# Performance work log

Measured on AMD Instinct MI355X. Metric: run time of the kernel, lower is better.

## Reference

```python
import jax, jax.numpy as jnp
import numpy as np

ALPHA = 0.34          # Ewald splitting parameter (init kwarg alpha)
MAX_HKL = 12          # init kwarg max_hkl
TWO_PI = 2.0 * np.pi


def setup_inputs() -> dict:
    key = jax.random.key(0)
    k1, k2 = jax.random.split(key)
    N = 4096
    L = 40.0  # cubic box edge (Angstrom)
    coords = jax.random.uniform(k1, (N, 3), dtype=jnp.float32) * L
    q = jax.random.normal(k2, (N,), dtype=jnp.float32)
    q = q - jnp.mean(q)  # neutral cell (k=0 term is excluded)
    box = jnp.eye(3, dtype=jnp.float32) * L
    return {"coords": coords, "box": box, "q": q}


def _ewald_recip_energy(coords, box, q):
    """Reciprocal-space Ewald sum over |h|,|k|,|l| <= MAX_HKL (rank=0 PME fallback).

    pot_i = (4*pi/V) * sum_{k!=0} exp(-|k|^2/(4 a^2))/|k|^2 * Re[S(k) exp(-i k.r_i)]
    E     = 0.5 * sum_i q_i * pot_i
    """
    K = MAX_HKL
    vol = jnp.abs(jnp.linalg.det(box))
    recip = TWO_PI * jnp.linalg.inv(box).T  # rows = reciprocal lattice vectors (3,3)
    h = jnp.arange(-K, K + 1)
    hh, kk, ll = jnp.meshgrid(h, h, h, indexing="ij")
    hkl = jnp.stack([hh.ravel(), kk.ravel(), ll.ravel()], axis=-1).astype(jnp.float32)  # (Nk,3)
    kvecs = hkl @ recip                      # (Nk,3)
    k2 = jnp.sum(kvecs * kvecs, axis=-1)     # (Nk,)
    nonzero = k2 > 0.0                       # mask out k = 0 (static shape, jit-safe)
    k2_safe = jnp.where(nonzero, k2, 1.0)
    inv_4a2 = 1.0 / (4.0 * ALPHA * ALPHA)
    fac = jnp.where(nonzero, jnp.exp(-k2_safe * inv_4a2) / k2_safe, 0.0)  # (Nk,)
    phases = coords @ kvecs.T                # (N, Nk)
    c = jnp.cos(phases)
    s = jnp.sin(phases)
    Sre = q @ c                              # (Nk,) Re S(k)
    Sim = q @ s                              # (Nk,) Im S(k)
    pref = (4.0 * np.pi) / vol
    # Re[S(k) e^{-i k.r_i}] = Sre*cos + Sim*sin
    pot = pref * (c @ (fac * Sre) + s @ (fac * Sim))  # (N,)
    return 0.5 * jnp.sum(q * pot)


def reference(coords, box, q):
    return _ewald_recip_energy(coords, box, q)
```

## Files before the change

kernel.cpp:

```cpp
#include <hip/hip_runtime.h>
#include <math.h>

namespace {
constexpr int   KMAX   = 12;
constexpr int   NLINE  = 313;
constexpr int   NGROUP = NLINE * 5;
constexpr int   NKV    = NGROUP * 5;
constexpr int   NSLICE = 4;
constexpr int   SLICE_CAP = 512;
constexpr int   S2_BLOCKS = (NKV + 255) / 256;
constexpr float ALPHA_  = 0.34f;
constexpr float TWO_PI_ = 6.283185307179586f;
}

__device__ __forceinline__ void cofactors(const float* __restrict__ box,
                                          float C[3][3], float* det) {
  const float b00 = box[0], b01 = box[1], b02 = box[2];
  const float b10 = box[3], b11 = box[4], b12 = box[5];
  const float b20 = box[6], b21 = box[7], b22 = box[8];
  C[0][0] =  (b11 * b22 - b12 * b21);
  C[0][1] = -(b10 * b22 - b12 * b20);
  C[0][2] =  (b10 * b21 - b11 * b20);
  C[1][0] = -(b01 * b22 - b02 * b21);
  C[1][1] =  (b00 * b22 - b02 * b20);
  C[1][2] = -(b00 * b21 - b01 * b20);
  C[2][0] =  (b01 * b12 - b02 * b11);
  C[2][1] = -(b00 * b12 - b02 * b10);
  C[2][2] =  (b00 * b11 - b01 * b10);
  *det = b00 * C[0][0] + b01 * C[0][1] + b02 * C[0][2];
}

__device__ __forceinline__ void line_hk(int L, int* h, int* k) {
  if (L < 300)      { *h = L / 25 + 1; *k = L % 25 - 12; }
  else if (L < 312) { *h = 0;          *k = L - 299;     }
  else              { *h = 0;          *k = 0;           }
}

__global__ __launch_bounds__(256, 6) void ewald_g5(
    const float* __restrict__ coords, const float* __restrict__ box,
    const float* __restrict__ q, int N, float2* __restrict__ partial)
{
  __shared__ float4 sf4[SLICE_CAP];
  __shared__ float2 sf2[SLICE_CAP];

  float C[3][3], det;
  cofactors(box, C, &det);
  const float invdet = 1.0f / det;

  const int slice = blockIdx.y;
  const int sp    = (N + NSLICE - 1) / NSLICE;
  const int s_beg = slice * sp;
  const int s_end = min(s_beg + sp, N);

  const int lane = threadIdx.x & 63;
  const int g    = blockIdx.x * 4 + (threadIdx.x >> 6);
  const int gc   = (g < NGROUP) ? g : (NGROUP - 1);

  int h, k; line_hk(gc / 5, &h, &k);
  const float hf  = (float)h;
  const float kf  = (float)k;
  const float l0f = (float)(-KMAX + 5 * (gc % 5));

  float Sre[5] = {0.f, 0.f, 0.f, 0.f, 0.f};
  float Sim[5] = {0.f, 0.f, 0.f, 0.f, 0.f};

  for (int cb = s_beg; cb < s_end; cb += SLICE_CAP) {
    const int cnt = min(SLICE_CAP, s_end - cb);
    __syncthreads();
    for (int t = threadIdx.x; t < SLICE_CAP; t += 256) {
      float4 v4 = make_float4(0.f, 0.f, 1.f, 0.f);
      float2 v2 = make_float2(0.f, 0.f);
      if (t < cnt) {
        const int gi = cb + t;
        const float x = coords[3 * gi + 0];
        const float y = coords[3 * gi + 1];
        const float z = coords[3 * gi + 2];
        v4.x = (x * C[0][0] + y * C[0][1] + z * C[0][2]) * invdet;
        v4.y = (x * C[1][0] + y * C[1][1] + z * C[1][2]) * invdet;
        float c = (x * C[2][0] + y * C[2][1] + z * C[2][2]) * invdet;
        c = c - floorf(c);
        float cr, sr;
        asm("v_sin_f32 %0, %1" : "=v"(sr) : "v"(c));
        asm("v_cos_f32 %0, %1" : "=v"(cr) : "v"(c));
        v4.z = cr; v4.w = sr;
        v2.x = c;  v2.y = q[gi];
      }
      sf4[t] = v4; sf2[t] = v2;
    }
    __syncthreads();

#pragma unroll 2
    for (int i = lane; i < SLICE_CAP; i += 64) {
      const float4 p = sf4[i];
      const float2 w = sf2[i];
      float t0 = fmaf(hf, p.x, fmaf(kf, p.y, l0f * w.x));
      float tf;
      asm("v_fract_f32 %0, %1" : "=v"(tf) : "v"(t0));
      float s0, c0;
      asm("v_sin_f32 %0, %1" : "=v"(s0) : "v"(tf));
      asm("v_cos_f32 %0, %1" : "=v"(c0) : "v"(tf));
      float Pre = w.y * c0, Pim = w.y * s0;
      Sre[0] += Pre; Sim[0] += Pim;
      const float cr = p.z, sr = p.w;
#pragma unroll
      for (int u = 1; u < 5; ++u) {
        const float nre = fmaf(Pre, cr, -(Pim * sr));
        const float nim = fmaf(Pre, sr,  (Pim * cr));
        Pre = nre; Pim = nim;
        Sre[u] += Pre; Sim[u] += Pim;
      }
    }
  }

#pragma unroll
  for (int off = 32; off > 0; off >>= 1) {
#pragma unroll
    for (int u = 0; u < 5; ++u) {
      Sre[u] += __shfl_xor(Sre[u], off);
      Sim[u] += __shfl_xor(Sim[u], off);
    }
  }

  if (g < NGROUP && lane == 0) {
#pragma unroll
    for (int u = 0; u < 5; ++u) {
      partial[(size_t)(g * 5 + u) * NSLICE + slice] = make_float2(Sre[u], Sim[u]);
    }
  }
}

__global__ __launch_bounds__(256) void stage2(
    const float2* __restrict__ partial, const float* __restrict__ box,
    float* __restrict__ out)
{
  __shared__ float red[256];
  const int idx = blockIdx.x * 256 + threadIdx.x;
  float e = 0.f;
  if (idx < NKV) {
    const int g = idx / 5, u = idx % 5;
    const int line = g / 5;
    const int l = -KMAX + 5 * (g % 5) + u;
    int h, k; line_hk(line, &h, &k);
    if (!(h == 0 && k == 0 && l <= 0)) {
      float re = 0.f, im = 0.f;
      for (int s = 0; s < NSLICE; ++s) {
        const float2 p = partial[(size_t)idx * NSLICE + s];
        re += p.x; im += p.y;
      }
      float C[3][3], det;
      cofactors(box, C, &det);
      const float invdet = 1.0f / det;
      const float hf = (float)h, kf = (float)k, lf = (float)l;
      const float kx = (hf * C[0][0] + kf * C[1][0] + lf * C[2][0]) * invdet;
      const float ky = (hf * C[0][1] + kf * C[1][1] + lf * C[2][1]) * invdet;
      const float kz = (hf * C[0][2] + kf * C[1][2] + lf * C[2][2]) * invdet;
      const float k2 = TWO_PI_ * TWO_PI_ * (kx * kx + ky * ky + kz * kz);
      const float fac = __expf(-k2 / (4.0f * ALPHA_ * ALPHA_)) / k2;
      e = fac * fmaf(re, re, im * im);
    }
  }
  red[threadIdx.x] = e;
  __syncthreads();
  for (int s = 128; s > 0; s >>= 1) {
    if (threadIdx.x < s) red[threadIdx.x] += red[threadIdx.x + s];
    __syncthreads();
  }
  if (threadIdx.x == 0) {
    float C[3][3], det;
    cofactors(box, C, &det);
    const float scale = (4.0f * 3.14159265358979323846f) / fabsf(det);
    atomicAdd(out, scale * red[0]);
  }
}

extern "C" void kernel_launch(void* const* d_in, const int* in_sizes, int n_in,
                              void* d_out, int out_size, void* d_ws, size_t ws_size,
                              hipStream_t stream) {
  const float* coords = (const float*)d_in[0];
  const float* box    = (const float*)d_in[1];
  const float* q      = (const float*)d_in[2];
  float* out = (float*)d_out;
  const int N = in_sizes[2];

  float2* partial = (float2*)d_ws;

  hipMemsetAsync(out, 0, sizeof(float), stream);
  const dim3 grid((NGROUP + 3) / 4, NSLICE);
  hipLaunchKernelGGL(ewald_g5, grid, dim3(256), 0, stream,
                     coords, box, q, N, partial);
  hipLaunchKernelGGL(stage2, dim3(S2_BLOCKS), dim3(256), 0, stream,
                     partial, box, out);
}
```

Before: 24.15 us.

## Map one k-group per thread with 128 atom slices, dropping wave reductions

The work split changes. Before, each wave handled one k-group over a quarter of the atoms and finished with a cross-lane shuffle reduction. Now each thread owns one k-group and each block handles a slice of 32 atoms, for 128 slices. Per-thread partials are written to the workspace, and stage2 reduces across the 128 slices using 4 lanes per k-vector. The hipMemsetAsync is replaced by an in-kernel zero of the output, which removes a launch but relies on the first kernel finishing before stage2's atomics. The cost is much more partial-sum traffic, about 128×7825 float2 values, plus a heavier stage2 reduction.

```diff
diff --git a/kernel.cpp b/kernel.cpp
--- a/kernel.cpp
+++ b/kernel.cpp
@@ -4,11 +4,13 @@
 namespace {
 constexpr int   KMAX   = 12;
 constexpr int   NLINE  = 313;
-constexpr int   NGROUP = NLINE * 5;
-constexpr int   NKV    = NGROUP * 5;
-constexpr int   NSLICE = 4;
-constexpr int   SLICE_CAP = 512;
-constexpr int   S2_BLOCKS = (NKV + 255) / 256;
+constexpr int   NL25   = 25;
+constexpr int   NKV    = NLINE * NL25;
+constexpr int   NG     = NLINE * 5;
+constexpr int   GPAD   = 7 * 256;
+constexpr int   NSLICE = 128;
+constexpr int   PART   = 32;
+constexpr int   S2_BLOCKS = (NKV * 4 + 255) / 256;
 constexpr float ALPHA_  = 0.34f;
 constexpr float TWO_PI_ = 6.283185307179586f;
 }
@@ -36,96 +38,79 @@
   else              { *h = 0;          *k = 0;           }
 }
 
-__global__ __launch_bounds__(256, 6) void ewald_g5(
+__global__ __launch_bounds__(256, 8) void ewald_t(
     const float* __restrict__ coords, const float* __restrict__ box,
-    const float* __restrict__ q, int N, float2* __restrict__ partial)
+    const float* __restrict__ q, int N, float2* __restrict__ partial,
+    float* __restrict__ out)
 {
-  __shared__ float4 sf4[SLICE_CAP];
-  __shared__ float2 sf2[SLICE_CAP];
-
-  float C[3][3], det;
-  cofactors(box, C, &det);
-  const float invdet = 1.0f / det;
+  __shared__ float4 sf4[PART];
+  __shared__ float2 sf2[PART];
 
   const int slice = blockIdx.y;
-  const int sp    = (N + NSLICE - 1) / NSLICE;
-  const int s_beg = slice * sp;
-  const int s_end = min(s_beg + sp, N);
+  if (blockIdx.x == 0 && slice == 0 && threadIdx.x == 0) out[0] = 0.0f;
 
-  const int lane = threadIdx.x & 63;
-  const int g    = blockIdx.x * 4 + (threadIdx.x >> 6);
-  const int gc   = (g < NGROUP) ? g : (NGROUP - 1);
+  if (threadIdx.x < PART) {
+    float C[3][3], det;
+    cofactors(box, C, &det);
+    const float invdet = 1.0f / det;
+    const int i = slice * PART + threadIdx.x;
+    float4 v4 = make_float4(0.f, 0.f, 1.f, 0.f);
+    float2 v2 = make_float2(0.f, 0.f);
+    if (i < N) {
+      const float x = coords[3 * i + 0];
+      const float y = coords[3 * i + 1];
+      const float z = coords[3 * i + 2];
+      v4.x = (x * C[0][0] + y * C[0][1] + z * C[0][2]) * invdet;
+      v4.y = (x * C[1][0] + y * C[1][1] + z * C[1][2]) * invdet;
+      float c = (x * C[2][0] + y * C[2][1] + z * C[2][2]) * invdet;
+      c = c - floorf(c);
+      float cr, sr;
+      asm("v_sin_f32 %0, %1" : "=v"(sr) : "v"(c));
+      asm("v_cos_f32 %0, %1" : "=v"(cr) : "v"(c));
+      v4.z = cr; v4.w = sr;
+      v2.x = c;  v2.y = q[i];
+    }
+    sf4[threadIdx.x] = v4;
+    sf2[threadIdx.x] = v2;
+  }
+  __syncthreads();
 
-  int h, k; line_hk(gc / 5, &h, &k);
+  const int gg  = blockIdx.x * 256 + threadIdx.x;
+  const int ggc = (gg < NG) ? gg : (NG - 1);
+  int h, k; line_hk(ggc / 5, &h, &k);
   const float hf  = (float)h;
   const float kf  = (float)k;
-  const float l0f = (float)(-KMAX + 5 * (gc % 5));
+  const float l0f = (float)(-KMAX + 5 * (ggc % 5));
 
   float Sre[5] = {0.f, 0.f, 0.f, 0.f, 0.f};
   float Sim[5] = {0.f, 0.f, 0.f, 0.f, 0.f};
 
-  for (int cb = s_beg; cb < s_end; cb += SLICE_CAP) {
-    const int cnt = min(SLICE_CAP, s_end - cb);
-    __syncthreads();
-    for (int t = threadIdx.x; t < SLICE_CAP; t += 256) {
-      float4 v4 = make_float4(0.f, 0.f, 1.f, 0.f);
-      float2 v2 = make_float2(0.f, 0.f);
-      if (t < cnt) {
-        const int gi = cb + t;
-        const float x = coords[3 * gi + 0];
-        const float y = coords[3 * gi + 1];
-        const float z = coords[3 * gi + 2];
-        v4.x = (x * C[0][0] + y * C[0][1] + z * C[0][2]) * invdet;
-        v4.y = (x * C[1][0] + y * C[1][1] + z * C[1][2]) * invdet;
-        float c = (x * C[2][0] + y * C[2][1] + z * C[2][2]) * invdet;
-        c = c - floorf(c);
-        float cr, sr;
-        asm("v_sin_f32 %0, %1" : "=v"(sr) : "v"(c));
-        asm("v_cos_f32 %0, %1" : "=v"(cr) : "v"(c));
-        v4.z = cr; v4.w = sr;
-        v2.x = c;  v2.y = q[gi];
-      }
-      sf4[t] = v4; sf2[t] = v2;
-    }
-    __syncthreads();
-
-#pragma unroll 2
-    for (int i = lane; i < SLICE_CAP; i += 64) {
-      const float4 p = sf4[i];
-      const float2 w = sf2[i];
-      float t0 = fmaf(hf, p.x, fmaf(kf, p.y, l0f * w.x));
-      float tf;
-      asm("v_fract_f32 %0, %1" : "=v"(tf) : "v"(t0));
-      float s0, c0;
-      asm("v_sin_f32 %0, %1" : "=v"(s0) : "v"(tf));
-      asm("v_cos_f32 %0, %1" : "=v"(c0) : "v"(tf));
-      float Pre = w.y * c0, Pim = w.y * s0;
-      Sre[0] += Pre; Sim[0] += Pim;
-      const float cr = p.z, sr = p.w;
+#pragma unroll 4
+  for (int j = 0; j < PART; ++j) {
+    const float4 p = sf4[j];
+    const float2 w = sf2[j];
+    float t0 = fmaf(hf, p.x, fmaf(kf, p.y, l0f * w.x));
+    float tf;
+    asm("v_fract_f32 %0, %1" : "=v"(tf) : "v"(t0));
+    float s0, c0;
+    asm("v_sin_f32 %0, %1" : "=v"(s0) : "v"(tf));
+    asm("v_cos_f32 %0, %1" : "=v"(c0) : "v"(tf));
+    float Pre = w.y * c0, Pim = w.y * s0;
+    Sre[0] += Pre; Sim[0] += Pim;
+    const float cr = p.z, sr = p.w;
 #pragma unroll
-      for (int u = 1; u < 5; ++u) {
-        const float nre = fmaf(Pre, cr, -(Pim * sr));
-        const float nim = fmaf(Pre, sr,  (Pim * cr));
-        Pre = nre; Pim = nim;
-        Sre[u] += Pre; Sim[u] += Pim;
-      }
+    for (int u = 1; u < 5; ++u) {
+      const float nre = fmaf(Pre, cr, -(Pim * sr));
+      const float nim = fmaf(Pre, sr,  (Pim * cr));
+      Pre = nre; Pim = nim;
+      Sre[u] += Pre; Sim[u] += Pim;
     }
   }
 
+  if (gg < NG) {
+    float2* dst = partial + ((size_t)slice * GPAD + gg) * 5;
 #pragma unroll
-  for (int off = 32; off > 0; off >>= 1) {
-#pragma unroll
-    for (int u = 0; u < 5; ++u) {
-      Sre[u] += __shfl_xor(Sre[u], off);
-      Sim[u] += __shfl_xor(Sim[u], off);
-    }
-  }
-
-  if (g < NGROUP && lane == 0) {
-#pragma unroll
-    for (int u = 0; u < 5; ++u) {
-      partial[(size_t)(g * 5 + u) * NSLICE + slice] = make_float2(Sre[u], Sim[u]);
-    }
+    for (int u = 0; u < 5; ++u) dst[u] = make_float2(Sre[u], Sim[u]);
   }
 }
 
@@ -134,30 +119,42 @@
     float* __restrict__ out)
 {
   __shared__ float red[256];
-  const int idx = blockIdx.x * 256 + threadIdx.x;
+  const int tid = blockIdx.x * 256 + threadIdx.x;
+  const int kv  = tid >> 2;
+  const int sq  = tid & 3;
+  float Sre = 0.f, Sim = 0.f;
+  bool valid = false;
+  int h = 0, k = 0, l = 0;
+  if (kv < NKV) {
+    const int L  = kv / NL25;
+    const int ls = kv % NL25;
+    l = ls - KMAX;
+    line_hk(L, &h, &k);
+    valid = !(h == 0 && k == 0 && l <= 0);
+    if (valid) {
+      const int g = L * 5 + ls / 5;
+      const int u = ls % 5;
+      for (int s = sq * 32; s < sq * 32 + 32; ++s) {
+        const float2 p = partial[((size_t)s * GPAD + g) * 5 + u];
+        Sre += p.x; Sim += p.y;
+      }
+    }
+  }
+  Sre += __shfl_xor(Sre, 1); Sre += __shfl_xor(Sre, 2);
+  Sim += __shfl_xor(Sim, 1); Sim += __shfl_xor(Sim, 2);
+
   float e = 0.f;
-  if (idx < NKV) {
-    const int g = idx / 5, u = idx % 5;
-    const int line = g / 5;
-    const int l = -KMAX + 5 * (g % 5) + u;
-    int h, k; line_hk(line, &h, &k);
-    if (!(h == 0 && k == 0 && l <= 0)) {
-      float re = 0.f, im = 0.f;
-      for (int s = 0; s < NSLICE; ++s) {
-        const float2 p = partial[(size_t)idx * NSLICE + s];
-        re += p.x; im += p.y;
-      }
-      float C[3][3], det;
-      cofactors(box, C, &det);
-      const float invdet = 1.0f / det;
-      const float hf = (float)h, kf = (float)k, lf = (float)l;
-      const float kx = (hf * C[0][0] + kf * C[1][0] + lf * C[2][0]) * invdet;
-      const float ky = (hf * C[0][1] + kf * C[1][1] + lf * C[2][1]) * invdet;
-      const float kz = (hf * C[0][2] + kf * C[1][2] + lf * C[2][2]) * invdet;
-      const float k2 = TWO_PI_ * TWO_PI_ * (kx * kx + ky * ky + kz * kz);
-      const float fac = __expf(-k2 / (4.0f * ALPHA_ * ALPHA_)) / k2;
-      e = fac * fmaf(re, re, im * im);
-    }
+  if (kv < NKV && valid && sq == 0) {
+    float C[3][3], det;
+    cofactors(box, C, &det);
+    const float invdet = 1.0f / det;
+    const float hf = (float)h, kf = (float)k, lf = (float)l;
+    const float kx = (hf * C[0][0] + kf * C[1][0] + lf * C[2][0]) * invdet;
+    const float ky = (hf * C[0][1] + kf * C[1][1] + lf * C[2][1]) * invdet;
+    const float kz = (hf * C[0][2] + kf * C[1][2] + lf * C[2][2]) * invdet;
+    const float k2 = TWO_PI_ * TWO_PI_ * (kx * kx + ky * ky + kz * kz);
+    const float fac = __expf(-k2 / (4.0f * ALPHA_ * ALPHA_)) / k2;
+    e = fac * fmaf(Sre, Sre, Sim * Sim);
   }
   red[threadIdx.x] = e;
   __syncthreads();
@@ -184,10 +181,8 @@
 
   float2* partial = (float2*)d_ws;
 
-  hipMemsetAsync(out, 0, sizeof(float), stream);
-  const dim3 grid((NGROUP + 3) / 4, NSLICE);
-  hipLaunchKernelGGL(ewald_g5, grid, dim3(256), 0, stream,
-                     coords, box, q, N, partial);
+  hipLaunchKernelGGL(ewald_t, dim3(7, NSLICE), dim3(256), 0, stream,
+                     coords, box, q, N, partial, out);
   hipLaunchKernelGGL(stage2, dim3(S2_BLOCKS), dim3(256), 0, stream,
                      partial, box, out);
 }
```

Result: faster. 23.04 us (-4.6%).
